# Performance work log

Measured on AMD Instinct MI355X. Metric: run time of the kernel, lower is better.

Reference implementation:

```python
import jax, jax.numpy as jnp
import numpy as np

B, C, N = 4, 64, 512
H = 128  # hidden width; MLP input is 2*C = 128


def setup_inputs() -> dict:
    key = jax.random.key(0)
    k0, k1, k2 = jax.random.split(key, 3)
    x = jax.random.normal(k0, (B, C, N), dtype=jnp.float32)
    # Torch Linear init ~ U(-1/sqrt(fan_in), 1/sqrt(fan_in)); stored as (in, out) for einsum.
    W1 = jax.random.normal(k1, (2 * C, H), dtype=jnp.float32) * (1.0 / np.sqrt(2 * C))
    b1 = jnp.zeros((H,), dtype=jnp.float32)
    W2 = jax.random.normal(k2, (H, 1), dtype=jnp.float32) * (1.0 / np.sqrt(H))
    b2 = jnp.zeros((1,), dtype=jnp.float32)
    return {"x": x, "W1": W1, "b1": b1, "W2": W2, "b2": b2}


def reference(x, W1, b1, W2, b2):
    # x: (B, C, N). Equivalent to the per-offset loop: for every pair (i, j) with
    # j > i, score = MLP(concat(x[:, :, i], x[:, :, j])), placed at y[:, i, j].
    # Dropout is identity in eval mode.
    b, c, n = x.shape
    xt = jnp.transpose(x, (0, 2, 1))                      # (B, N, C)
    left = jnp.broadcast_to(xt[:, :, None, :], (b, n, n, c))   # row index i
    right = jnp.broadcast_to(xt[:, None, :, :], (b, n, n, c))  # col index j
    pairs = jnp.concatenate([left, right], axis=-1)       # (B, N, N, 2C)
    h = jax.nn.relu(jnp.einsum('bijc,ch->bijh', pairs, W1) + b1)
    score = (jnp.einsum('bijh,ho->bijo', h, W2) + b2)[..., 0]  # (B, N, N)
    mask = jnp.triu(jnp.ones((n, n), dtype=score.dtype), k=1)  # strict upper triangle
    return score * mask
```

## Files before the change

### kernel.cpp

```cpp
#include <hip/hip_runtime.h>

#define B_ 4
#define C_ 64
#define N_ 512
#define H_ 128

__global__ __launch_bounds__(256) void proj_kernel(
    const float* __restrict__ x, const float* __restrict__ W1,
    const float* __restrict__ b1, float* __restrict__ Lbuf,
    float* __restrict__ Rbuf)
{
    __shared__ float Wl[64 * 128];
    __shared__ float xs[16 * 68];

    const int t    = threadIdx.x;
    const int half = blockIdx.x >> 7;
    const int rem  = blockIdx.x & 127;
    const int b    = rem >> 5;
    const int i0   = (rem & 31) * 16;
    const int cbase = half * 64;

    const float4* W14 = (const float4*)W1;
    float4* Wl4 = (float4*)Wl;
    #pragma unroll
    for (int k = 0; k < 8; ++k)
        Wl4[t + k * 256] = W14[cbase * 32 + t + k * 256];

    #pragma unroll
    for (int k = 0; k < 4; ++k) {
        int idx = t + k * 256;
        int c = idx >> 4, ii = idx & 15;
        xs[ii * 68 + c] = x[b * (C_ * N_) + c * N_ + i0 + ii];
    }
    __syncthreads();

    const int hq  = t & 31;
    const int il  = (t >> 5) * 2;
    const int col = hq * 4;

    float4 a0, a1;
    if (half) { a0 = *(const float4*)(b1 + col); a1 = a0; }
    else      { a0 = make_float4(0.f, 0.f, 0.f, 0.f); a1 = a0; }

    #pragma unroll
    for (int c = 0; c < 64; c += 4) {
        float4 xv0 = *(float4*)(xs + il * 68 + c);
        float4 xv1 = *(float4*)(xs + (il + 1) * 68 + c);
        const float* x0p = (const float*)&xv0;
        const float* x1p = (const float*)&xv1;
        #pragma unroll
        for (int cc = 0; cc < 4; ++cc) {
            float4 w = Wl4[(c + cc) * 32 + hq];
            a0.x = fmaf(w.x, x0p[cc], a0.x);
            a0.y = fmaf(w.y, x0p[cc], a0.y);
            a0.z = fmaf(w.z, x0p[cc], a0.z);
            a0.w = fmaf(w.w, x0p[cc], a0.w);
            a1.x = fmaf(w.x, x1p[cc], a1.x);
            a1.y = fmaf(w.y, x1p[cc], a1.y);
            a1.z = fmaf(w.z, x1p[cc], a1.z);
            a1.w = fmaf(w.w, x1p[cc], a1.w);
        }
    }

    float* buf = half ? Rbuf : Lbuf;
    float* o = buf + b * (N_ * H_) + (i0 + il) * H_ + col;
    *(float4*)o = a0;
    *(float4*)(o + H_) = a1;
}

__global__ __launch_bounds__(64) void pair_kernel(
    const float* __restrict__ Lbuf, const float* __restrict__ Rbuf,
    const float* __restrict__ W2, const float* __restrict__ b2,
    float* __restrict__ out)
{
    __shared__ float4 Lt4[32 * 32];
    __shared__ float4 Rt4[32 * 32];

    const int t    = threadIdx.x;
    const int b    = blockIdx.x >> 8;
    const int tile = blockIdx.x & 255;
    const int ti0  = (tile >> 4) * 32;
    const int tj0  = (tile & 15) * 32;

    float* outb = out + b * (N_ * N_);

    if (tj0 + 31 <= ti0) {
        float4 z = make_float4(0.f, 0.f, 0.f, 0.f);
        #pragma unroll
        for (int k = 0; k < 4; ++k) {
            int idx = t + k * 64;
            int r = idx >> 3, cq = idx & 7;
            *(float4*)(outb + (ti0 + r) * N_ + tj0 + cq * 4) = z;
        }
        return;
    }

    const float* Lsrc = Lbuf + b * (N_ * H_) + ti0 * H_;
    const float* Rsrc = Rbuf + b * (N_ * H_) + tj0 * H_;
    #pragma unroll
    for (int k = 0; k < 16; ++k) {
        int idx = t + k * 64;
        int row = idx >> 5, hc = idx & 31;
        int sc = hc ^ (row >> 2);
        Lt4[row * 32 + sc] = *(const float4*)(Lsrc + idx * 4);
        Rt4[row * 32 + sc] = *(const float4*)(Rsrc + idx * 4);
    }
    __syncthreads();

    const int gL  = t >> 3;
    const int gR  = t & 7;
    const int til = gL * 4, tjl = gR * 4;

    float acc[4][4];
    #pragma unroll
    for (int r = 0; r < 4; ++r)
        #pragma unroll
        for (int c = 0; c < 4; ++c) acc[r][c] = 0.f;

    const float4* W24 = (const float4*)W2;

    #pragma unroll 2
    for (int hc = 0; hc < 32; ++hc) {
        const int scL = hc ^ gL;
        const int scR = hc ^ gR;
        float4 Lr[4], Rc[4];
        #pragma unroll
        for (int r = 0; r < 4; ++r) Lr[r] = Lt4[(til + r) * 32 + scL];
        #pragma unroll
        for (int c = 0; c < 4; ++c) Rc[c] = Rt4[(tjl + c) * 32 + scR];
        float4 wv = W24[hc];
        const float* wp = (const float*)&wv;
        #pragma unroll
        for (int r = 0; r < 4; ++r) {
            const float* lp = (const float*)&Lr[r];
            #pragma unroll
            for (int c = 0; c < 4; ++c) {
                const float* rp = (const float*)&Rc[c];
                float s = acc[r][c];
                #pragma unroll
                for (int k = 0; k < 4; ++k) {
                    float v = fmaxf(lp[k] + rp[k], 0.f);
                    s = fmaf(v, wp[k], s);
                }
                acc[r][c] = s;
            }
        }
    }

    const float bias2 = b2[0];
    #pragma unroll
    for (int r = 0; r < 4; ++r) {
        const int gi = ti0 + til + r;
        float4 v;
        float* vp = (float*)&v;
        #pragma unroll
        for (int c = 0; c < 4; ++c) {
            const int gj = tj0 + tjl + c;
            vp[c] = (gj > gi) ? (acc[r][c] + bias2) : 0.f;
        }
        *(float4*)(outb + gi * N_ + tj0 + tjl) = v;
    }
}

extern "C" void kernel_launch(void* const* d_in, const int* in_sizes, int n_in,
                              void* d_out, int out_size, void* d_ws, size_t ws_size,
                              hipStream_t stream)
{
    const float* x  = (const float*)d_in[0];
    const float* W1 = (const float*)d_in[1];
    const float* b1 = (const float*)d_in[2];
    const float* W2 = (const float*)d_in[3];
    const float* b2 = (const float*)d_in[4];
    float* out  = (float*)d_out;
    float* Lbuf = (float*)d_ws;
    float* Rbuf = Lbuf + B_ * N_ * H_;

    proj_kernel<<<256, 256, 0, stream>>>(x, W1, b1, Lbuf, Rbuf);
    pair_kernel<<<B_ * 256, 64, 0, stream>>>(Lbuf, Rbuf, W2, b2, out);
}
```

Before: 81.39 us.

## Split pair kernel hidden reduction across four waves with shared-memory reduce

The pair kernel now runs 256 threads per block: each of four waves handles a quarter of the hidden dimension for the same 32x32 output tile, and the partial sums are combined through shared memory before masking and storing. The aim is more waves per tile and more latency hiding, given only 1024 blocks of a single wave before. This adds two barriers and a shared-memory reduction stage, and reuses the L tile buffer as scratch for the reduction.

```diff
diff --git a/kernel.cpp b/kernel.cpp
--- a/kernel.cpp
+++ b/kernel.cpp
@@ -68,7 +68,7 @@
     *(float4*)(o + H_) = a1;
 }
 
-__global__ __launch_bounds__(64) void pair_kernel(
+__global__ __launch_bounds__(256) void pair_kernel(
     const float* __restrict__ Lbuf, const float* __restrict__ Rbuf,
     const float* __restrict__ W2, const float* __restrict__ b2,
     float* __restrict__ out)
@@ -85,21 +85,17 @@
     float* outb = out + b * (N_ * N_);
 
     if (tj0 + 31 <= ti0) {
-        float4 z = make_float4(0.f, 0.f, 0.f, 0.f);
-        #pragma unroll
-        for (int k = 0; k < 4; ++k) {
-            int idx = t + k * 64;
-            int r = idx >> 3, cq = idx & 7;
-            *(float4*)(outb + (ti0 + r) * N_ + tj0 + cq * 4) = z;
-        }
+        int r = t >> 3, cq = t & 7;
+        *(float4*)(outb + (ti0 + r) * N_ + tj0 + cq * 4) =
+            make_float4(0.f, 0.f, 0.f, 0.f);
         return;
     }
 
     const float* Lsrc = Lbuf + b * (N_ * H_) + ti0 * H_;
     const float* Rsrc = Rbuf + b * (N_ * H_) + tj0 * H_;
     #pragma unroll
-    for (int k = 0; k < 16; ++k) {
-        int idx = t + k * 64;
+    for (int k = 0; k < 4; ++k) {
+        int idx = t + k * 256;
         int row = idx >> 5, hc = idx & 31;
         int sc = hc ^ (row >> 2);
         Lt4[row * 32 + sc] = *(const float4*)(Lsrc + idx * 4);
@@ -107,9 +103,12 @@
     }
     __syncthreads();
 
-    const int gL  = t >> 3;
-    const int gR  = t & 7;
-    const int til = gL * 4, tjl = gR * 4;
+    const int wave = t >> 6;
+    const int lane = t & 63;
+    const int gL   = lane >> 3;
+    const int gR   = lane & 7;
+    const int til  = gL * 4, tjl = gR * 4;
+    const int hc0  = wave * 8;
 
     float acc[4][4];
     #pragma unroll
@@ -119,8 +118,9 @@
 
     const float4* W24 = (const float4*)W2;
 
-    #pragma unroll 2
-    for (int hc = 0; hc < 32; ++hc) {
+    #pragma unroll
+    for (int k8 = 0; k8 < 8; ++k8) {
+        const int hc  = hc0 + k8;
         const int scL = hc ^ gL;
         const int scR = hc ^ gR;
         float4 Lr[4], Rc[4];
@@ -147,18 +147,30 @@
         }
     }
 
-    const float bias2 = b2[0];
+    __syncthreads();
+    float4* redq = Lt4;
     #pragma unroll
-    for (int r = 0; r < 4; ++r) {
-        const int gi = ti0 + til + r;
+    for (int r = 0; r < 4; ++r)
+        redq[wave * 256 + (til + r) * 8 + gR] =
+            make_float4(acc[r][0], acc[r][1], acc[r][2], acc[r][3]);
+    __syncthreads();
+
+    {
+        const int r  = t >> 3;
+        const int cq = t & 7;
+        float4 s0 = redq[r * 8 + cq];
+        float4 s1 = redq[256 + r * 8 + cq];
+        float4 s2 = redq[512 + r * 8 + cq];
+        float4 s3 = redq[768 + r * 8 + cq];
+        const float bias2 = b2[0];
+        const int gi = ti0 + r;
+        const int gj0 = tj0 + cq * 4;
         float4 v;
-        float* vp = (float*)&v;
-        #pragma unroll
-        for (int c = 0; c < 4; ++c) {
-            const int gj = tj0 + tjl + c;
-            vp[c] = (gj > gi) ? (acc[r][c] + bias2) : 0.f;
-        }
-        *(float4*)(outb + gi * N_ + tj0 + tjl) = v;
+        v.x = (gj0     > gi) ? (s0.x + s1.x + s2.x + s3.x + bias2) : 0.f;
+        v.y = (gj0 + 1 > gi) ? (s0.y + s1.y + s2.y + s3.y + bias2) : 0.f;
+        v.z = (gj0 + 2 > gi) ? (s0.z + s1.z + s2.z + s3.z + bias2) : 0.f;
+        v.w = (gj0 + 3 > gi) ? (s0.w + s1.w + s2.w + s3.w + bias2) : 0.f;
+        *(float4*)(outb + gi * N_ + gj0) = v;
     }
 }
 
@@ -176,5 +188,5 @@
     float* Rbuf = Lbuf + B_ * N_ * H_;
 
     proj_kernel<<<256, 256, 0, stream>>>(x, W1, b1, Lbuf, Rbuf);
-    pair_kernel<<<B_ * 256, 64, 0, stream>>>(Lbuf, Rbuf, W2, b2, out);
+    pair_kernel<<<B_ * 256, 256, 0, stream>>>(Lbuf, Rbuf, W2, b2, out);
 }
```

Result: faster. 78.40 us (-3.7%).
